# Kernel optimization log

Hardware: AMD Instinct MI355X
Metric: run time of the kernel (lower is better)

The kernel has to match this reference:

```python
import jax, jax.numpy as jnp
import numpy as np

F = 128      # n_features
NRBF = 6     # radial basis size
NSH = 7      # spherical basis size (SbfLayer(N_shbf, N_shbf, c))
NBIL = 8     # bilinear dim
CUT = 5.0    # cutoff c
NA = 4096    # atoms
NE = 65536   # edges
NT = 262144  # triplets
NB = 64      # molecules in batch
NZ = 95      # atom types


def _swish(x):
    return x * jax.nn.sigmoid(x)


def setup_inputs():
    key = jax.random.key(0)
    ks = list(jax.random.split(key, 32))
    def nrm(k, shape, s):
        return jax.random.normal(k, shape, dtype=jnp.float32) * s
    inp = {}
    inp['Z'] = jax.random.randint(ks[0], (NA,), 0, NZ)
    inp['R'] = jax.random.normal(ks[1], (NA, 3), dtype=jnp.float32)
    inp['batch_seg'] = jnp.sort(jax.random.randint(ks[2], (NA,), 0, NB))
    inp['idnb_i'] = jax.random.randint(ks[3], (NE,), 0, NA)
    inp['idnb_j'] = jax.random.randint(ks[4], (NE,), 0, NA)
    inp['id_expand_kj'] = jax.random.randint(ks[5], (NT,), 0, NE)
    inp['id_reduce_ji'] = jax.random.randint(ks[6], (NT,), 0, NE)
    inp['id3dnb_i'] = jax.random.randint(ks[7], (NT,), 0, NA)
    inp['id3dnb_j'] = jax.random.randint(ks[8], (NT,), 0, NA)
    inp['id3dnb_k'] = jax.random.randint(ks[9], (NT,), 0, NA)
    # learned parameters
    inp['emb'] = nrm(ks[10], (NZ, F), 0.1)
    inp['W_emb'] = nrm(ks[11], (2 * F + NRBF, F), 0.05)
    inp['b_emb'] = jnp.zeros((F,), jnp.float32)
    inp['out_Wrbf'] = nrm(ks[12], (8, NRBF, F), 0.05)
    inp['out_W1'] = nrm(ks[13], (8, F, F), 0.05)
    inp['out_b1'] = jnp.zeros((8, F), jnp.float32)
    inp['out_W2'] = nrm(ks[14], (8, F, 1), 0.05)
    inp['int_Wrbf'] = nrm(ks[15], (7, NRBF, F), 0.05)
    inp['int_Wsbf'] = nrm(ks[16], (7, NSH * NSH, NBIL), 0.05)
    inp['int_Wkj'] = nrm(ks[17], (7, F, F), 0.05)
    inp['int_bkj'] = jnp.zeros((7, F), jnp.float32)
    inp['int_Wji'] = nrm(ks[18], (7, F, F), 0.05)
    inp['int_bji'] = jnp.zeros((7, F), jnp.float32)
    inp['int_Wbil'] = nrm(ks[19], (7, F, NBIL, F), 0.02)
    inp['int_Wfin'] = nrm(ks[20], (7, F, F), 0.05)
    inp['int_bfin'] = jnp.zeros((7, F), jnp.float32)
    return inp


def _forward(Z, R, batch_seg, idnb_i, idnb_j, id_expand_kj, id_reduce_ji,
             id3dnb_i, id3dnb_j, id3dnb_k,
             emb, W_emb, b_emb,
             out_Wrbf, out_W1, out_b1, out_W2,
             int_Wrbf, int_Wsbf, int_Wkj, int_bkj, int_Wji, int_bji,
             int_Wbil, int_Wfin, int_bfin):
    n_atoms = Z.shape[0]
    n_edges = idnb_i.shape[0]
    # interatomic distances Dij [E]
    diff = R[idnb_i] - R[idnb_j]
    Dij = jnp.sqrt(jax.nn.relu(jnp.sum(diff * diff, -1)))
    dsafe = jnp.maximum(Dij, 1e-6)
    # radial Bessel basis [E, NRBF]
    n = jnp.arange(1, NRBF + 1, dtype=R.dtype)
    rbf = jnp.sqrt(2.0 / CUT) * jnp.sin(n * jnp.pi * dsafe[:, None] / CUT) / dsafe[:, None]
    # triplet angles via cross/atan2 [T]
    R1 = R[id3dnb_j] - R[id3dnb_i]
    R2 = R[id3dnb_k] - R[id3dnb_i]
    x = jnp.sum(R1 * R2, -1)
    y = jnp.linalg.norm(jnp.cross(R1, R2), axis=-1)
    ang = jnp.arctan2(y, x)
    # spherical basis: radial(d_kj) x angular(cos(l*theta)) -> [T, NSH*NSH]
    d_kj = jnp.maximum(Dij[id_expand_kj], 1e-6)
    nr = jnp.arange(1, NSH + 1, dtype=R.dtype)
    radial = jnp.sin(nr * jnp.pi * d_kj[:, None] / CUT) / d_kj[:, None]       # [T, NSH]
    ls = jnp.arange(NSH, dtype=R.dtype)
    angular = jnp.cos(ls[None, :] * ang[:, None])                              # [T, NSH]
    sbf = (angular[:, :, None] * radial[:, None, :]).reshape(ang.shape[0], NSH * NSH)
    # embedding: edge messages m [E, F]
    h = emb[Z]
    m = _swish(jnp.concatenate([h[idnb_i], h[idnb_j], rbf], -1) @ W_emb + b_emb)

    def out_layer(m, k):
        t = m * (rbf @ out_Wrbf[k])                                            # [E, F]
        ta = jax.ops.segment_sum(t, idnb_i, num_segments=n_atoms)             # [A, F]
        ta = _swish(ta @ out_W1[k] + out_b1[k])
        return ta @ out_W2[k]                                                  # [A, 1]

    P = out_layer(m, 0)
    for i in range(7):
        x_ji = _swish(m @ int_Wji[i] + int_bji[i])
        x_kj = _swish(m @ int_Wkj[i] + int_bkj[i]) * (rbf @ int_Wrbf[i])       # [E, F]
        x_kj = x_kj[id_expand_kj]                                              # [T, F]
        sb = sbf @ int_Wsbf[i]                                                 # [T, NBIL]
        x_kj = jnp.einsum('wl,wj,jli->wi', sb, x_kj, int_Wbil[i])             # [T, F]
        x_kj = jax.ops.segment_sum(x_kj, id_reduce_ji, num_segments=n_edges)  # [E, F]
        m = m + _swish((x_ji + x_kj) @ int_Wfin[i] + int_bfin[i])
        P = P + out_layer(m, i + 1)
    return jax.ops.segment_sum(P, batch_seg, num_segments=NB)                 # [NB, 1]


def reference(Z, R, batch_seg, idnb_i, idnb_j, id_expand_kj, id_reduce_ji,
              id3dnb_i, id3dnb_j, id3dnb_k,
              emb, W_emb, b_emb,
              out_Wrbf, out_W1, out_b1, out_W2,
              int_Wrbf, int_Wsbf, int_Wkj, int_bkj, int_Wji, int_bji,
              int_Wbil, int_Wfin, int_bfin):
    return _forward(Z, R, batch_seg, idnb_i, idnb_j, id_expand_kj, id_reduce_ji,
                    id3dnb_i, id3dnb_j, id3dnb_k,
                    emb, W_emb, b_emb,
                    out_Wrbf, out_W1, out_b1, out_W2,
                    int_Wrbf, int_Wsbf, int_Wkj, int_bkj, int_Wji, int_bji,
                    int_Wbil, int_Wfin, int_bfin)
```

## Files before the change

### kernel.cpp

```cpp
#include <hip/hip_runtime.h>

typedef __attribute__((ext_vector_type(8))) short shortx8;
typedef __attribute__((ext_vector_type(4))) float floatx4;

constexpr int NAc = 4096;
constexpr int NEc = 65536;
constexpr int NTc = 262144;
constexpr float PI_F = 3.14159265358979323846f;
constexpr float SQ25 = 0.63245553203367587f;

__device__ __forceinline__ float bf2f(unsigned short h){ return __uint_as_float(((unsigned)h)<<16); }
__device__ __forceinline__ unsigned short f2bf(float f){
  unsigned u = __float_as_uint(f);
  u += 0x7fffu + ((u>>16)&1u);
  return (unsigned short)(u>>16);
}
__device__ __forceinline__ float swishf(float x){ return x/(1.f+__expf(-x)); }

__device__ __forceinline__ floatx4 mfma16x16x32bf(shortx8 a, shortx8 b, floatx4 c){
  floatx4 d;
  asm("v_mfma_f32_16x16x32_bf16 %0, %1, %2, %3" : "=v"(d) : "v"(a), "v"(b), "v"(c));
  return d;
}

__global__ __launch_bounds__(256)
void egeom_k(const float* __restrict__ R, const int* __restrict__ ei,
             const int* __restrict__ ej, float* __restrict__ Dij, float* __restrict__ rbf){
  int e = blockIdx.x*256 + threadIdx.x;
  int i = ei[e], j = ej[e];
  float dx = R[i*3+0]-R[j*3+0];
  float dy = R[i*3+1]-R[j*3+1];
  float dz = R[i*3+2]-R[j*3+2];
  float d2 = dx*dx+dy*dy+dz*dz;
  float D = sqrtf(fmaxf(d2, 0.f));
  Dij[e] = D;
  float d = fmaxf(D, 1e-6f);
  float s = PI_F*d*0.2f;
  float sn, cs; sincosf(s, &sn, &cs);
  float invd = SQ25/d;
  float sprev = 0.f, scur = sn;
  #pragma unroll
  for (int q=0;q<6;q++){
    rbf[e*6+q] = scur*invd;
    float nx = 2.f*cs*scur - sprev; sprev = scur; scur = nx;
  }
}

__global__ __launch_bounds__(256)
void tgeom_k(const float* __restrict__ R, const int* __restrict__ t3i,
             const int* __restrict__ t3j, const int* __restrict__ t3k,
             const int* __restrict__ texp, const float* __restrict__ Dij,
             float* __restrict__ angrad){
  int w = blockIdx.x*256 + threadIdx.x;
  int ia = t3i[w], ja = t3j[w], ka = t3k[w];
  float xi = R[ia*3+0], yi = R[ia*3+1], zi = R[ia*3+2];
  float r1x = R[ja*3+0]-xi, r1y = R[ja*3+1]-yi, r1z = R[ja*3+2]-zi;
  float r2x = R[ka*3+0]-xi, r2y = R[ka*3+1]-yi, r2z = R[ka*3+2]-zi;
  float dt = r1x*r2x + r1y*r2y + r1z*r2z;
  float cx = r1y*r2z - r1z*r2y;
  float cy = r1z*r2x - r1x*r2z;
  float cz = r1x*r2y - r1y*r2x;
  float yv = sqrtf(cx*cx + cy*cy + cz*cz);
  float h = sqrtf(dt*dt + yv*yv);
  float c1 = (h > 0.f) ? dt/h : 1.f;
  angrad[0*NTc + w] = 1.f;
  angrad[1*NTc + w] = c1;
  float cprev = 1.f, ccur = c1;
  #pragma unroll
  for (int l=2;l<7;l++){
    float nx = 2.f*c1*ccur - cprev; cprev = ccur; ccur = nx;
    angrad[l*NTc + w] = nx;
  }
  float d = fmaxf(Dij[texp[w]], 1e-6f);
  float s = PI_F*d*0.2f;
  float sn, cs; sincosf(s, &sn, &cs);
  float invd = 1.f/d;
  float sprev = 0.f, scur = sn;
  #pragma unroll
  for (int q=0;q<7;q++){
    angrad[(7+q)*NTc + w] = scur*invd;
    float nx = 2.f*cs*scur - sprev; sprev = scur; scur = nx;
  }
}

__global__ __launch_bounds__(256)
void prep_transpose(const float* __restrict__ Wemb, const float* __restrict__ Wji,
                    const float* __restrict__ Wkj, const float* __restrict__ Wfin,
                    unsigned short* __restrict__ dW12, unsigned short* __restrict__ dWji,
                    unsigned short* __restrict__ dWkj, unsigned short* __restrict__ dWfin){
  int y = blockIdx.y;
  int x = blockIdx.x*256 + threadIdx.x;
  if (y == 0){
    if (x < 32768){
      int n = x >> 8, k = x & 255;
      dW12[x] = f2bf(Wemb[k*128 + n]);
    }
  } else {
    if (x < 16384){
      int n = x >> 7, k = x & 127;
      const float* s; unsigned short* d;
      if (y <= 7)      { s = Wji  + (y-1)*16384;  d = dWji  + (y-1)*16384; }
      else if (y <= 14){ s = Wkj  + (y-8)*16384;  d = dWkj  + (y-8)*16384; }
      else             { s = Wfin + (y-15)*16384; d = dWfin + (y-15)*16384; }
      d[x] = f2bf(s[k*128 + n]);
    }
  }
}

__global__ __launch_bounds__(256)
void prep_wbil(const float* __restrict__ Wbil, unsigned short* __restrict__ dst){
  int x = blockIdx.x*256 + threadIdx.x;
  if (x < 7*131072){
    int i = x >> 17; int rem = x & 131071;
    int o = rem >> 10; int lj = rem & 1023;
    int l = lj >> 7; int j = lj & 127;
    dst[x] = f2bf(Wbil[(size_t)i*131072 + (size_t)(j*8+l)*128 + o]);
  }
}

__global__ __launch_bounds__(256)
void prep_emb(const float* __restrict__ emb, unsigned short* __restrict__ d){
  int x = blockIdx.x*256 + threadIdx.x;
  if (x < 95*128) d[x] = f2bf(emb[x]);
}

__global__ __launch_bounds__(256)
void hist_k(const int* __restrict__ ids, int n, int* __restrict__ hist){
  int stride = gridDim.x*blockDim.x;
  for (int x = blockIdx.x*blockDim.x + threadIdx.x; x < n; x += stride)
    atomicAdd(&hist[ids[x]], 1);
}

__global__ __launch_bounds__(1024)
void scan_k(const int* __restrict__ hist, int* __restrict__ offs, int nbins){
  __shared__ int part[1024];
  int tid = threadIdx.x;
  int per = nbins >> 10;
  int base = tid*per;
  int s = 0;
  for (int q=0;q<per;q++) s += hist[base+q];
  part[tid] = s;
  __syncthreads();
  for (int d=1; d<1024; d<<=1){
    int v = (tid>=d) ? part[tid-d] : 0;
    __syncthreads();
    part[tid] += v;
    __syncthreads();
  }
  int run = (tid>0) ? part[tid-1] : 0;
  for (int q=0;q<per;q++){ offs[base+q] = run; run += hist[base+q]; }
  if (tid==1023) offs[nbins] = part[1023];
}

__global__ __launch_bounds__(256)
void scatter_k(const int* __restrict__ ids, int n, const int* __restrict__ offs,
               int* __restrict__ cursor, int* __restrict__ perm){
  int stride = gridDim.x*blockDim.x;
  for (int x = blockIdx.x*blockDim.x + threadIdx.x; x < n; x += stride){
    int b = ids[x];
    int pos = offs[b] + atomicAdd(&cursor[b], 1);
    perm[pos] = x;
  }
}

__global__ __launch_bounds__(256)
void sb_k(const float* __restrict__ angrad, const float* __restrict__ Wsbf,
          float* __restrict__ sb){
  __shared__ float Ws[392];
  for (int x = threadIdx.x; x < 392; x += 256) Ws[x] = Wsbf[x];
  __syncthreads();
  int w = blockIdx.x*256 + threadIdx.x;
  float ca[7], rd[7];
  #pragma unroll
  for (int q=0;q<7;q++){ ca[q] = angrad[q*NTc + w]; rd[q] = angrad[(7+q)*NTc + w]; }
  float o[8] = {0,0,0,0,0,0,0,0};
  #pragma unroll
  for (int a=0;a<7;a++){
    #pragma unroll
    for (int r=0;r<7;r++){
      float pr = ca[a]*rd[r];
      const float* wp = &Ws[(a*7+r)*8];
      #pragma unroll
      for (int l=0;l<8;l++) o[l] += pr*wp[l];
    }
  }
  #pragma unroll
  for (int l=0;l<8;l++) sb[(size_t)w*8 + l] = o[l];
}

__global__ __launch_bounds__(256)
void gbuild_k(int c0, const int* __restrict__ tperm, const int* __restrict__ toffs,
              const int* __restrict__ texp, const float* __restrict__ sb,
              const unsigned short* __restrict__ xkj, unsigned short* __restrict__ G){
  int lane = threadIdx.x & 63;
  int wv = threadIdx.x >> 6;
  int r = c0 + blockIdx.x*4 + wv;
  float acc[8][2] = {};
  int s = toffs[r], e_ = toffs[r+1];
  for (int t = s; t < e_; t++){
    int wt = tperm[t];
    int e = texp[wt];
    unsigned xv = *(const unsigned*)&xkj[(size_t)e*128 + lane*2];
    float x0 = bf2f((unsigned short)(xv & 0xffffu));
    float x1 = bf2f((unsigned short)(xv >> 16));
    const float* sp = sb + (size_t)wt*8;
    #pragma unroll
    for (int l=0;l<8;l++){ float sl = sp[l]; acc[l][0] += sl*x0; acc[l][1] += sl*x1; }
  }
  size_t gb = (size_t)(r - c0)*1024 + lane*2;
  #pragma unroll
  for (int l=0;l<8;l++){
    unsigned pv = (unsigned)f2bf(acc[l][0]) | ((unsigned)f2bf(acc[l][1]) << 16);
    *(unsigned*)&G[gb + l*128] = pv;
  }
}

template<int MODE, int EPI>
__global__ __launch_bounds__(256)
void gemm_k(const unsigned short* __restrict__ A, const unsigned short* __restrict__ Bt,
            int K, int rowoff, int arow0,
            const int* __restrict__ gi, const int* __restrict__ gj, const int* __restrict__ Zr,
            const float* __restrict__ rbfp, const float* __restrict__ W6,
            const float* __restrict__ bias, const float* minp,
            const unsigned short* __restrict__ xjip,
            float* outF, unsigned short* outB){
  __shared__ __align__(16) unsigned short As[128*72];
  __shared__ __align__(16) unsigned short Bs[128*72];
  const int tid = threadIdx.x;
  const int lane = tid & 63;
  const int wid = tid >> 6;
  const int wr = wid >> 1, wc = wid & 1;
  const int rowbase = rowoff + blockIdx.x*128;
  floatx4 acc[4][4];
  #pragma unroll
  for (int i=0;i<4;i++)
    #pragma unroll
    for (int j=0;j<4;j++) acc[i][j] = (floatx4){0.f,0.f,0.f,0.f};

  for (int k0 = 0; k0 < K; k0 += 64){
    shortx8 ra[4], rb[4];
    #pragma unroll
    for (int q=0;q<4;q++){
      int c = q*256 + tid;
      int row = c >> 3;
      int ko = (c & 7) << 3;
      const unsigned short* asrc;
      if (MODE == 0){
        asrc = A + (size_t)(rowbase - arow0 + row)*K + k0 + ko;
      } else {
        int grow = rowbase + row;
        int kg = k0 + ko;
        int atom = (kg < 128) ? gi[grow] : gj[grow];
        asrc = A + (size_t)Zr[atom]*128 + (kg & 127);
      }
      ra[q] = *(const shortx8*)asrc;
      rb[q] = *(const shortx8*)(Bt + (size_t)row*K + k0 + ko);
    }
    __syncthreads();
    #pragma unroll
    for (int q=0;q<4;q++){
      int c = q*256 + tid;
      int row = c >> 3;
      int ko = (c & 7) << 3;
      *(shortx8*)&As[row*72 + ko] = ra[q];
      *(shortx8*)&Bs[row*72 + ko] = rb[q];
    }
    __syncthreads();
    #pragma unroll
    for (int kk=0; kk<2; kk++){
      shortx8 af[4], bfr[4];
      #pragma unroll
      for (int mi=0;mi<4;mi++)
        af[mi] = *(const shortx8*)&As[(wr*64 + mi*16 + (lane&15))*72 + kk*32 + ((lane>>4)<<3)];
      #pragma unroll
      for (int ni=0;ni<4;ni++)
        bfr[ni] = *(const shortx8*)&Bs[(wc*64 + ni*16 + (lane&15))*72 + kk*32 + ((lane>>4)<<3)];
      #pragma unroll
      for (int mi=0;mi<4;mi++)
        #pragma unroll
        for (int ni=0;ni<4;ni++)
          acc[mi][ni] = mfma16x16x32bf(af[mi], bfr[ni], acc[mi][ni]);
    }
  }
  asm volatile("s_nop 7\ns_nop 7\ns_nop 7");

  #pragma unroll
  for (int mi=0;mi<4;mi++){
    #pragma unroll
    for (int j=0;j<4;j++){
      int row = wr*64 + mi*16 + ((lane>>4)<<2) + j;
      int grow = rowbase + row;
      float rb6[6];
      if (EPI==0 || EPI==2){
        #pragma unroll
        for (int q=0;q<6;q++) rb6[q] = rbfp[grow*6+q];
      }
      #pragma unroll
      for (int ni=0;ni<4;ni++){
        int col = wc*64 + ni*16 + (lane&15);
        float v = acc[mi][ni][j];
        size_t oidx = (size_t)grow*128 + col;
        if (EPI==0){
          float e = bias[col];
          #pragma unroll
          for (int q=0;q<6;q++) e += rb6[q]*W6[q*128+col];
          v = swishf(v + e);
          outF[oidx] = v;
          outB[oidx] = f2bf(v);
        } else if (EPI==1){
          v = swishf(v + bias[col]);
          outB[oidx] = f2bf(v);
        } else if (EPI==2){
          float rp = 0.f;
          #pragma unroll
          for (int q=0;q<6;q++) rp += rb6[q]*W6[q*128+col];
          v = swishf(v + bias[col]) * rp;
          outB[oidx] = f2bf(v);
        } else if (EPI==3){
          v += bf2f(xjip[oidx]);
          outB[oidx] = f2bf(v);
        } else {
          float nm = minp[oidx] + swishf(v + bias[col]);
          outF[oidx] = nm;
          outB[oidx] = f2bf(nm);
        }
      }
    }
  }
}

__global__ __launch_bounds__(256)
void out_layer_k(const int* __restrict__ eperm, const int* __restrict__ eoffs,
                 const unsigned short* __restrict__ mbf, const float* __restrict__ rbf,
                 const float* __restrict__ Wrbf, const float* __restrict__ W1,
                 const float* __restrict__ b1, const float* __restrict__ W2,
                 const int* __restrict__ bseg, float* __restrict__ out){
  __shared__ float ta_lds[4][128];
  int lane = threadIdx.x & 63;
  int wv = threadIdx.x >> 6;
  int a = blockIdx.x*4 + wv;
  int f0 = lane*2;
  float wr0[6], wr1[6];
  #pragma unroll
  for (int q=0;q<6;q++){ wr0[q] = Wrbf[q*128+f0]; wr1[q] = Wrbf[q*128+f0+1]; }
  float ta0 = 0.f, ta1 = 0.f;
  int s = eoffs[a], e_ = eoffs[a+1];
  for (int t = s; t < e_; t++){
    int e = eperm[t];
    unsigned mv = *(const unsigned*)&mbf[(size_t)e*128 + f0];
    float r0 = rbf[e*6+0], r1 = rbf[e*6+1], r2 = rbf[e*6+2];
    float r3 = rbf[e*6+3], r4 = rbf[e*6+4], r5 = rbf[e*6+5];
    float rp0 = r0*wr0[0]+r1*wr0[1]+r2*wr0[2]+r3*wr0[3]+r4*wr0[4]+r5*wr0[5];
    float rp1 = r0*wr1[0]+r1*wr1[1]+r2*wr1[2]+r3*wr1[3]+r4*wr1[4]+r5*wr1[5];
    ta0 += bf2f((unsigned short)(mv & 0xffffu))*rp0;
    ta1 += bf2f((unsigned short)(mv >> 16))*rp1;
  }
  ta_lds[wv][f0]   = ta0;
  ta_lds[wv][f0+1] = ta1;
  float p = 0.f;
  #pragma unroll
  for (int h=0; h<2; h++){
    int n = lane + h*64;
    float o = b1[n];
    for (int f=0; f<128; f++) o += ta_lds[wv][f]*W1[f*128+n];
    p += swishf(o)*W2[n];
  }
  #pragma unroll
  for (int off=32; off; off>>=1) p += __shfl_down(p, off);
  if (lane == 0) atomicAdd(&out[bseg[a]], p);
}

extern "C" void kernel_launch(void* const* d_in, const int* in_sizes, int n_in,
                              void* d_out, int out_size, void* d_ws, size_t ws_size,
                              hipStream_t stream){
  const int*   Z    = (const int*)d_in[0];
  const float* R    = (const float*)d_in[1];
  const int*   bseg = (const int*)d_in[2];
  const int*   ei   = (const int*)d_in[3];
  const int*   ej   = (const int*)d_in[4];
  const int*   texp = (const int*)d_in[5];
  const int*   tred = (const int*)d_in[6];
  const int*   t3i  = (const int*)d_in[7];
  const int*   t3j  = (const int*)d_in[8];
  const int*   t3k  = (const int*)d_in[9];
  const float* emb  = (const float*)d_in[10];
  const float* Wemb = (const float*)d_in[11];
  const float* bemb = (const float*)d_in[12];
  const float* oWr  = (const float*)d_in[13];
  const float* oW1  = (const float*)d_in[14];
  const float* ob1  = (const float*)d_in[15];
  const float* oW2  = (const float*)d_in[16];
  const float* iWr  = (const float*)d_in[17];
  const float* iWs  = (const float*)d_in[18];
  const float* iWkj = (const float*)d_in[19];
  const float* ibkj = (const float*)d_in[20];
  const float* iWji = (const float*)d_in[21];
  const float* ibji = (const float*)d_in[22];
  const float* iWb  = (const float*)d_in[23];
  const float* iWf  = (const float*)d_in[24];
  const float* ibf  = (const float*)d_in[25];
  float* out = (float*)d_out;

  char* p = (char*)d_ws;
  auto alloc = [&](size_t bytes)->char*{ char* r = p; p += (bytes + 255) & ~(size_t)255; return r; };
  float* Dij    = (float*)alloc((size_t)NEc*4);
  float* rbf    = (float*)alloc((size_t)NEc*6*4);
  float* angrad = (float*)alloc((size_t)14*NTc*4);
  float* sball  = (float*)alloc((size_t)NTc*8*4);
  float* m      = (float*)alloc((size_t)NEc*128*4);
  unsigned short* mbf  = (unsigned short*)alloc((size_t)NEc*128*2);
  unsigned short* xji  = (unsigned short*)alloc((size_t)NEc*128*2);
  unsigned short* xkj  = (unsigned short*)alloc((size_t)NEc*128*2);
  unsigned short* afin = (unsigned short*)alloc((size_t)NEc*128*2);
  int* thist = (int*)alloc((size_t)NEc*4);
  int* toffs = (int*)alloc((size_t)(NEc+1)*4);
  int* tperm = (int*)alloc((size_t)NTc*4);
  int* ehist = (int*)alloc((size_t)NAc*4);
  int* eoffs = (int*)alloc((size_t)(NAc+1)*4);
  int* eperm = (int*)alloc((size_t)NEc*4);
  unsigned short* embbf = (unsigned short*)alloc((size_t)95*128*2);
  unsigned short* W12et = (unsigned short*)alloc((size_t)128*256*2);
  unsigned short* Wjit  = (unsigned short*)alloc((size_t)7*16384*2);
  unsigned short* Wkjt  = (unsigned short*)alloc((size_t)7*16384*2);
  unsigned short* Wfint = (unsigned short*)alloc((size_t)7*16384*2);
  unsigned short* Wbilt = (unsigned short*)alloc((size_t)7*131072*2);
  size_t fixed = (size_t)(p - (char*)d_ws);

  int nch = 1;
  while (nch < 8 && fixed + ((size_t)NEc/nch)*1024*2 > ws_size) nch <<= 1;
  int ECH = NEc / nch;
  unsigned short* Gbuf = (unsigned short*)alloc((size_t)ECH*1024*2);

  hipMemsetAsync(d_out, 0, 64*sizeof(float), stream);
  hipMemsetAsync(thist, 0, (size_t)NEc*4, stream);
  hipMemsetAsync(ehist, 0, (size_t)NAc*4, stream);

  prep_transpose<<<dim3(128,22),256,0,stream>>>(Wemb, iWji, iWkj, iWf, W12et, Wjit, Wkjt, Wfint);
  prep_wbil<<<3584,256,0,stream>>>(iWb, Wbilt);
  prep_emb<<<48,256,0,stream>>>(emb, embbf);
  egeom_k<<<NEc/256,256,0,stream>>>(R, ei, ej, Dij, rbf);
  tgeom_k<<<NTc/256,256,0,stream>>>(R, t3i, t3j, t3k, texp, Dij, angrad);

  hist_k<<<512,256,0,stream>>>(tred, NTc, thist);
  scan_k<<<1,1024,0,stream>>>(thist, toffs, NEc);
  hipMemsetAsync(thist, 0, (size_t)NEc*4, stream);
  scatter_k<<<512,256,0,stream>>>(tred, NTc, toffs, thist, tperm);
  hist_k<<<256,256,0,stream>>>(ei, NEc, ehist);
  scan_k<<<1,1024,0,stream>>>(ehist, eoffs, NAc);
  hipMemsetAsync(ehist, 0, (size_t)NAc*4, stream);
  scatter_k<<<256,256,0,stream>>>(ei, NEc, eoffs, ehist, eperm);

  gemm_k<1,0><<<NEc/128,256,0,stream>>>(embbf, W12et, 256, 0, 0, ei, ej, Z,
                                        rbf, Wemb + 256*128, bemb, nullptr, nullptr, m, mbf);
  out_layer_k<<<NAc/4,256,0,stream>>>(eperm, eoffs, mbf, rbf,
                                      oWr, oW1, ob1, oW2, bseg, out);

  for (int i=0;i<7;i++){
    sb_k<<<NTc/256,256,0,stream>>>(angrad, iWs + i*392, sball);
    gemm_k<0,1><<<NEc/128,256,0,stream>>>(mbf, Wjit + i*16384, 128, 0, 0,
        nullptr, nullptr, nullptr, nullptr, nullptr, ibji + i*128, nullptr, nullptr, nullptr, xji);
    gemm_k<0,2><<<NEc/128,256,0,stream>>>(mbf, Wkjt + i*16384, 128, 0, 0,
        nullptr, nullptr, nullptr, rbf, iWr + i*768, ibkj + i*128, nullptr, nullptr, nullptr, xkj);
    for (int c=0;c<nch;c++){
      int c0 = c*ECH;
      gbuild_k<<<ECH/4,256,0,stream>>>(c0, tperm, toffs, texp, sball, xkj, Gbuf);
      gemm_k<0,3><<<ECH/128,256,0,stream>>>(Gbuf, Wbilt + i*131072, 1024, c0, c0,
          nullptr, nullptr, nullptr, nullptr, nullptr, nullptr, nullptr, xji, nullptr, afin);
    }
    gemm_k<0,4><<<NEc/128,256,0,stream>>>(afin, Wfint + i*16384, 128, 0, 0,
        nullptr, nullptr, nullptr, nullptr, nullptr, ibf + i*128, m, nullptr, m, mbf);
    out_layer_k<<<NAc/4,256,0,stream>>>(eperm, eoffs, mbf, rbf,
        oWr + (i+1)*768, oW1 + (i+1)*16384, ob1 + (i+1)*128, oW2 + (i+1)*128, bseg, out);
  }
  (void)in_sizes; (void)n_in; (void)out_size;
}
```

Measured before the change: 1.789 ms.

## Pre-permute triplet data, merge ji/kj GEMMs, parallelize scan, vectorize gbuild stores

Triplet angular features and expand indices are gathered once into reduce-sorted order, so sb_k and gbuild_k read contiguously instead of through tperm indirection. The ji and kj projection GEMMs are merged into one launch with a 2D grid over a concatenated weight. The single-block scan is replaced by a three-kernel multi-block scan. The G layout changes to lane-contiguous 16-element vectors with matching Wbil reordering so stores are 128-bit. These target indirect gathers, launch count and serial scan cost, at the price of extra buffers and a one-time permutation pass.

Result: slower. 1.871 ms (+4.6%).

```diff
diff --git a/kernel.cpp b/kernel.cpp
--- a/kernel.cpp
+++ b/kernel.cpp
@@ -2,6 +2,7 @@
 
 typedef __attribute__((ext_vector_type(8))) short shortx8;
 typedef __attribute__((ext_vector_type(4))) float floatx4;
+typedef __attribute__((ext_vector_type(4))) unsigned uintx4;
 
 constexpr int NAc = 4096;
 constexpr int NEc = 65536;
@@ -86,8 +87,8 @@
 __global__ __launch_bounds__(256)
 void prep_transpose(const float* __restrict__ Wemb, const float* __restrict__ Wji,
                     const float* __restrict__ Wkj, const float* __restrict__ Wfin,
-                    unsigned short* __restrict__ dW12, unsigned short* __restrict__ dWji,
-                    unsigned short* __restrict__ dWkj, unsigned short* __restrict__ dWfin){
+                    unsigned short* __restrict__ dW12, unsigned short* __restrict__ dWjk,
+                    unsigned short* __restrict__ dWfin){
   int y = blockIdx.y;
   int x = blockIdx.x*256 + threadIdx.x;
   if (y == 0){
@@ -99,8 +100,8 @@
     if (x < 16384){
       int n = x >> 7, k = x & 127;
       const float* s; unsigned short* d;
-      if (y <= 7)      { s = Wji  + (y-1)*16384;  d = dWji  + (y-1)*16384; }
-      else if (y <= 14){ s = Wkj  + (y-8)*16384;  d = dWkj  + (y-8)*16384; }
+      if (y <= 7)      { s = Wji  + (y-1)*16384;  d = dWjk  + (y-1)*32768; }
+      else if (y <= 14){ s = Wkj  + (y-8)*16384;  d = dWjk  + (y-8)*32768 + 16384; }
       else             { s = Wfin + (y-15)*16384; d = dWfin + (y-15)*16384; }
       d[x] = f2bf(s[k*128 + n]);
     }
@@ -112,9 +113,8 @@
   int x = blockIdx.x*256 + threadIdx.x;
   if (x < 7*131072){
     int i = x >> 17; int rem = x & 131071;
-    int o = rem >> 10; int lj = rem & 1023;
-    int l = lj >> 7; int j = lj & 127;
-    dst[x] = f2bf(Wbil[(size_t)i*131072 + (size_t)(j*8+l)*128 + o]);
+    int o = rem >> 10; int k = rem & 1023;
+    dst[x] = f2bf(Wbil[(size_t)i*131072 + (size_t)k*128 + o]);
   }
 }
 
@@ -131,25 +131,43 @@
     atomicAdd(&hist[ids[x]], 1);
 }
 
-__global__ __launch_bounds__(1024)
-void scan_k(const int* __restrict__ hist, int* __restrict__ offs, int nbins){
-  __shared__ int part[1024];
-  int tid = threadIdx.x;
-  int per = nbins >> 10;
-  int base = tid*per;
-  int s = 0;
-  for (int q=0;q<per;q++) s += hist[base+q];
-  part[tid] = s;
-  __syncthreads();
-  for (int d=1; d<1024; d<<=1){
-    int v = (tid>=d) ? part[tid-d] : 0;
-    __syncthreads();
-    part[tid] += v;
-    __syncthreads();
-  }
-  int run = (tid>0) ? part[tid-1] : 0;
-  for (int q=0;q<per;q++){ offs[base+q] = run; run += hist[base+q]; }
-  if (tid==1023) offs[nbins] = part[1023];
+__global__ __launch_bounds__(256)
+void scan1_k(const int* __restrict__ hist, int* __restrict__ offs, int* __restrict__ bsum){
+  __shared__ int buf[256];
+  int t = threadIdx.x;
+  int x = blockIdx.x*256 + t;
+  int v = hist[x];
+  buf[t] = v; __syncthreads();
+  #pragma unroll
+  for (int d=1; d<256; d<<=1){
+    int u = (t>=d) ? buf[t-d] : 0;
+    __syncthreads(); buf[t] += u; __syncthreads();
+  }
+  offs[x] = buf[t] - v;
+  if (t == 255) bsum[blockIdx.x] = buf[255];
+}
+
+__global__ __launch_bounds__(256)
+void scan2_k(int* __restrict__ bsum, int nb){
+  __shared__ int buf[256];
+  int t = threadIdx.x;
+  int v = (t < nb) ? bsum[t] : 0;
+  buf[t] = v; __syncthreads();
+  #pragma unroll
+  for (int d=1; d<256; d<<=1){
+    int u = (t>=d) ? buf[t-d] : 0;
+    __syncthreads(); buf[t] += u; __syncthreads();
+  }
+  if (t < nb) bsum[t] = buf[t] - v;
+}
+
+__global__ __launch_bounds__(256)
+void scan3_k(const int* __restrict__ hist, int* __restrict__ offs,
+             const int* __restrict__ bsum, int nbins){
+  int x = blockIdx.x*256 + threadIdx.x;
+  int o = offs[x] + bsum[blockIdx.x];
+  offs[x] = o;
+  if (x == nbins-1) offs[nbins] = o + hist[x];
 }
 
 __global__ __launch_bounds__(256)
@@ -164,15 +182,27 @@
 }
 
 __global__ __launch_bounds__(256)
-void sb_k(const float* __restrict__ angrad, const float* __restrict__ Wsbf,
+void permt_k(const int* __restrict__ tperm, const int* __restrict__ texp,
+             const float* __restrict__ angrad, int* __restrict__ tmeta,
+             float* __restrict__ angp){
+  int p = blockIdx.x*256 + threadIdx.x;
+  int w = tperm[p];
+  tmeta[p] = texp[w];
+  #pragma unroll
+  for (int q=0;q<14;q++) angp[(size_t)p*16 + q] = angrad[q*NTc + w];
+}
+
+__global__ __launch_bounds__(256)
+void sb_k(const float* __restrict__ angp, const float* __restrict__ Wsbf,
           float* __restrict__ sb){
   __shared__ float Ws[392];
   for (int x = threadIdx.x; x < 392; x += 256) Ws[x] = Wsbf[x];
   __syncthreads();
-  int w = blockIdx.x*256 + threadIdx.x;
-  float ca[7], rd[7];
-  #pragma unroll
-  for (int q=0;q<7;q++){ ca[q] = angrad[q*NTc + w]; rd[q] = angrad[(7+q)*NTc + w]; }
+  int p = blockIdx.x*256 + threadIdx.x;
+  const float4* ap = (const float4*)(angp + (size_t)p*16);
+  float4 a0 = ap[0], a1 = ap[1], a2 = ap[2], a3 = ap[3];
+  float ca[7] = {a0.x,a0.y,a0.z,a0.w,a1.x,a1.y,a1.z};
+  float rd[7] = {a1.w,a2.x,a2.y,a2.z,a2.w,a3.x,a3.y};
   float o[8] = {0,0,0,0,0,0,0,0};
   #pragma unroll
   for (int a=0;a<7;a++){
@@ -184,35 +214,45 @@
       for (int l=0;l<8;l++) o[l] += pr*wp[l];
     }
   }
-  #pragma unroll
-  for (int l=0;l<8;l++) sb[(size_t)w*8 + l] = o[l];
-}
-
-__global__ __launch_bounds__(256)
-void gbuild_k(int c0, const int* __restrict__ tperm, const int* __restrict__ toffs,
-              const int* __restrict__ texp, const float* __restrict__ sb,
-              const unsigned short* __restrict__ xkj, unsigned short* __restrict__ G){
+  float4* op = (float4*)(sb + (size_t)p*8);
+  op[0] = (float4){o[0],o[1],o[2],o[3]};
+  op[1] = (float4){o[4],o[5],o[6],o[7]};
+}
+
+__global__ __launch_bounds__(256)
+void gbuild_k(int c0, const int* __restrict__ toffs, const int* __restrict__ tmeta,
+              const float* __restrict__ sb, const unsigned short* __restrict__ xkj,
+              unsigned short* __restrict__ G){
   int lane = threadIdx.x & 63;
-  int wv = threadIdx.x >> 6;
+  int wv = __builtin_amdgcn_readfirstlane(threadIdx.x >> 6);
   int r = c0 + blockIdx.x*4 + wv;
-  float acc[8][2] = {};
+  float acc0[8] = {}, acc1[8] = {};
   int s = toffs[r], e_ = toffs[r+1];
   for (int t = s; t < e_; t++){
-    int wt = tperm[t];
-    int e = texp[wt];
+    int e = tmeta[t];
     unsigned xv = *(const unsigned*)&xkj[(size_t)e*128 + lane*2];
+    float4 s0 = *(const float4*)&sb[(size_t)t*8];
+    float4 s1 = *(const float4*)&sb[(size_t)t*8 + 4];
     float x0 = bf2f((unsigned short)(xv & 0xffffu));
     float x1 = bf2f((unsigned short)(xv >> 16));
-    const float* sp = sb + (size_t)wt*8;
-    #pragma unroll
-    for (int l=0;l<8;l++){ float sl = sp[l]; acc[l][0] += sl*x0; acc[l][1] += sl*x1; }
-  }
-  size_t gb = (size_t)(r - c0)*1024 + lane*2;
-  #pragma unroll
-  for (int l=0;l<8;l++){
-    unsigned pv = (unsigned)f2bf(acc[l][0]) | ((unsigned)f2bf(acc[l][1]) << 16);
-    *(unsigned*)&G[gb + l*128] = pv;
-  }
+    acc0[0] += s0.x*x0; acc1[0] += s0.x*x1;
+    acc0[1] += s0.y*x0; acc1[1] += s0.y*x1;
+    acc0[2] += s0.z*x0; acc1[2] += s0.z*x1;
+    acc0[3] += s0.w*x0; acc1[3] += s0.w*x1;
+    acc0[4] += s1.x*x0; acc1[4] += s1.x*x1;
+    acc0[5] += s1.y*x0; acc1[5] += s1.y*x1;
+    acc0[6] += s1.z*x0; acc1[6] += s1.z*x1;
+    acc0[7] += s1.w*x0; acc1[7] += s1.w*x1;
+  }
+  size_t base = (size_t)(r - c0)*1024 + (size_t)lane*16;
+  uintx4 v0, v1;
+  #pragma unroll
+  for (int d=0; d<4; d++){
+    v0[d] = (unsigned)f2bf(acc0[2*d]) | ((unsigned)f2bf(acc0[2*d+1]) << 16);
+    v1[d] = (unsigned)f2bf(acc1[2*d]) | ((unsigned)f2bf(acc1[2*d+1]) << 16);
+  }
+  *(uintx4*)&G[base]     = v0;
+  *(uintx4*)&G[base + 8] = v1;
 }
 
 template<int MODE, int EPI>
@@ -221,9 +261,9 @@
             int K, int rowoff, int arow0,
             const int* __restrict__ gi, const int* __restrict__ gj, const int* __restrict__ Zr,
             const float* __restrict__ rbfp, const float* __restrict__ W6,
-            const float* __restrict__ bias, const float* minp,
-            const unsigned short* __restrict__ xjip,
-            float* outF, unsigned short* outB){
+            const float* __restrict__ bias, const float* __restrict__ bias2,
+            const float* minp, const unsigned short* __restrict__ xjip,
+            float* outF, unsigned short* outB, unsigned short* outB2){
   __shared__ __align__(16) unsigned short As[128*72];
   __shared__ __align__(16) unsigned short Bs[128*72];
   const int tid = threadIdx.x;
@@ -231,6 +271,7 @@
   const int wid = tid >> 6;
   const int wr = wid >> 1, wc = wid & 1;
   const int rowbase = rowoff + blockIdx.x*128;
+  const int brow0 = (EPI==5) ? (int)blockIdx.y*128 : 0;
   floatx4 acc[4][4];
   #pragma unroll
   for (int i=0;i<4;i++)
@@ -254,7 +295,7 @@
         asrc = A + (size_t)Zr[atom]*128 + (kg & 127);
       }
       ra[q] = *(const shortx8*)asrc;
-      rb[q] = *(const shortx8*)(Bt + (size_t)row*K + k0 + ko);
+      rb[q] = *(const shortx8*)(Bt + (size_t)(brow0 + row)*K + k0 + ko);
     }
     __syncthreads();
     #pragma unroll
@@ -291,7 +332,8 @@
       int row = wr*64 + mi*16 + ((lane>>4)<<2) + j;
       int grow = rowbase + row;
       float rb6[6];
-      if (EPI==0 || EPI==2){
+      bool needr = (EPI==0) || ((EPI==5) && blockIdx.y==1);
+      if (needr){
         #pragma unroll
         for (int q=0;q<6;q++) rb6[q] = rbfp[grow*6+q];
       }
@@ -307,22 +349,24 @@
           v = swishf(v + e);
           outF[oidx] = v;
           outB[oidx] = f2bf(v);
-        } else if (EPI==1){
-          v = swishf(v + bias[col]);
-          outB[oidx] = f2bf(v);
-        } else if (EPI==2){
-          float rp = 0.f;
-          #pragma unroll
-          for (int q=0;q<6;q++) rp += rb6[q]*W6[q*128+col];
-          v = swishf(v + bias[col]) * rp;
-          outB[oidx] = f2bf(v);
         } else if (EPI==3){
           v += bf2f(xjip[oidx]);
           outB[oidx] = f2bf(v);
-        } else {
+        } else if (EPI==4){
           float nm = minp[oidx] + swishf(v + bias[col]);
           outF[oidx] = nm;
           outB[oidx] = f2bf(nm);
+        } else {
+          if (blockIdx.y == 0){
+            v = swishf(v + bias[col]);
+            outB[oidx] = f2bf(v);
+          } else {
+            float rp = 0.f;
+            #pragma unroll
+            for (int q=0;q<6;q++) rp += rb6[q]*W6[q*128+col];
+            v = swishf(v + bias2[col]) * rp;
+            outB2[oidx] = f2bf(v);
+          }
         }
       }
     }
@@ -337,7 +381,7 @@
                  const int* __restrict__ bseg, float* __restrict__ out){
   __shared__ float ta_lds[4][128];
   int lane = threadIdx.x & 63;
-  int wv = threadIdx.x >> 6;
+  int wv = __builtin_amdgcn_readfirstlane(threadIdx.x >> 6);
   int a = blockIdx.x*4 + wv;
   int f0 = lane*2;
   float wr0[6], wr1[6];
@@ -406,6 +450,7 @@
   float* Dij    = (float*)alloc((size_t)NEc*4);
   float* rbf    = (float*)alloc((size_t)NEc*6*4);
   float* angrad = (float*)alloc((size_t)14*NTc*4);
+  float* angp   = (float*)alloc((size_t)NTc*16*4);
   float* sball  = (float*)alloc((size_t)NTc*8*4);
   float* m      = (float*)alloc((size_t)NEc*128*4);
   unsigned short* mbf  = (unsigned short*)alloc((size_t)NEc*128*2);
@@ -415,13 +460,14 @@
   int* thist = (int*)alloc((size_t)NEc*4);
   int* toffs = (int*)alloc((size_t)(NEc+1)*4);
   int* tperm = (int*)alloc((size_t)NTc*4);
+  int* tmeta = (int*)alloc((size_t)NTc*4);
   int* ehist = (int*)alloc((size_t)NAc*4);
   int* eoffs = (int*)alloc((size_t)(NAc+1)*4);
   int* eperm = (int*)alloc((size_t)NEc*4);
+  int* bsum  = (int*)alloc((size_t)257*4);
   unsigned short* embbf = (unsigned short*)alloc((size_t)95*128*2);
   unsigned short* W12et = (unsigned short*)alloc((size_t)128*256*2);
-  unsigned short* Wjit  = (unsigned short*)alloc((size_t)7*16384*2);
-  unsigned short* Wkjt  = (unsigned short*)alloc((size_t)7*16384*2);
+  unsigned short* Wjkt  = (unsigned short*)alloc((size_t)7*32768*2);
   unsigned short* Wfint = (unsigned short*)alloc((size_t)7*16384*2);
   unsigned short* Wbilt = (unsigned short*)alloc((size_t)7*131072*2);
   size_t fixed = (size_t)(p - (char*)d_ws);
@@ -435,40 +481,46 @@
   hipMemsetAsync(thist, 0, (size_t)NEc*4, stream);
   hipMemsetAsync(ehist, 0, (size_t)NAc*4, stream);
 
-  prep_transpose<<<dim3(128,22),256,0,stream>>>(Wemb, iWji, iWkj, iWf, W12et, Wjit, Wkjt, Wfint);
+  prep_transpose<<<dim3(128,22),256,0,stream>>>(Wemb, iWji, iWkj, iWf, W12et, Wjkt, Wfint);
   prep_wbil<<<3584,256,0,stream>>>(iWb, Wbilt);
   prep_emb<<<48,256,0,stream>>>(emb, embbf);
   egeom_k<<<NEc/256,256,0,stream>>>(R, ei, ej, Dij, rbf);
   tgeom_k<<<NTc/256,256,0,stream>>>(R, t3i, t3j, t3k, texp, Dij, angrad);
 
   hist_k<<<512,256,0,stream>>>(tred, NTc, thist);
-  scan_k<<<1,1024,0,stream>>>(thist, toffs, NEc);
+  scan1_k<<<NEc/256,256,0,stream>>>(thist, toffs, bsum);
+  scan2_k<<<1,256,0,stream>>>(bsum, NEc/256);
+  scan3_k<<<NEc/256,256,0,stream>>>(thist, toffs, bsum, NEc);
   hipMemsetAsync(thist, 0, (size_t)NEc*4, stream);
   scatter_k<<<512,256,0,stream>>>(tred, NTc, toffs, thist, tperm);
   hist_k<<<256,256,0,stream>>>(ei, NEc, ehist);
-  scan_k<<<1,1024,0,stream>>>(ehist, eoffs, NAc);
+  scan1_k<<<NAc/256,256,0,stream>>>(ehist, eoffs, bsum);
+  scan2_k<<<1,256,0,stream>>>(bsum, NAc/256);
+  scan3_k<<<NAc/256,256,0,stream>>>(ehist, eoffs, bsum, NAc);
   hipMemsetAsync(ehist, 0, (size_t)NAc*4, stream);
   scatter_k<<<256,256,0,stream>>>(ei, NEc, eoffs, ehist, eperm);
+  permt_k<<<NTc/256,256,0,stream>>>(tperm, texp, angrad, tmeta, angp);
 
   gemm_k<1,0><<<NEc/128,256,0,stream>>>(embbf, W12et, 256, 0, 0, ei, ej, Z,
-                                        rbf, Wemb + 256*128, bemb, nullptr, nullptr, m, mbf);
+      rbf, Wemb + 256*128, bemb, nullptr, nullptr, nullptr, m, mbf, nullptr);
   out_layer_k<<<NAc/4,256,0,stream>>>(eperm, eoffs, mbf, rbf,
                                       oWr, oW1, ob1, oW2, bseg, out);
 
   for (int i=0;i<7;i++){
-    sb_k<<<NTc/256,256,0,stream>>>(angrad, iWs + i*392, sball);
-    gemm_k<0,1><<<NEc/128,256,0,stream>>>(mbf, Wjit + i*16384, 128, 0, 0,
-        nullptr, nullptr, nullptr, nullptr, nullptr, ibji + i*128, nullptr, nullptr, nullptr, xji);
-    gemm_k<0,2><<<NEc/128,256,0,stream>>>(mbf, Wkjt + i*16384, 128, 0, 0,
-        nullptr, nullptr, nullptr, rbf, iWr + i*768, ibkj + i*128, nullptr, nullptr, nullptr, xkj);
+    sb_k<<<NTc/256,256,0,stream>>>(angp, iWs + i*392, sball);
+    gemm_k<0,5><<<dim3(NEc/128,2),256,0,stream>>>(mbf, Wjkt + i*32768, 128, 0, 0,
+        nullptr, nullptr, nullptr, rbf, iWr + i*768, ibji + i*128, ibkj + i*128,
+        nullptr, nullptr, nullptr, xji, xkj);
     for (int c=0;c<nch;c++){
       int c0 = c*ECH;
-      gbuild_k<<<ECH/4,256,0,stream>>>(c0, tperm, toffs, texp, sball, xkj, Gbuf);
+      gbuild_k<<<ECH/4,256,0,stream>>>(c0, toffs, tmeta, sball, xkj, Gbuf);
       gemm_k<0,3><<<ECH/128,256,0,stream>>>(Gbuf, Wbilt + i*131072, 1024, c0, c0,
-          nullptr, nullptr, nullptr, nullptr, nullptr, nullptr, nullptr, xji, nullptr, afin);
+          nullptr, nullptr, nullptr, nullptr, nullptr, nullptr, nullptr, nullptr,
+          xji, nullptr, afin, nullptr);
     }
     gemm_k<0,4><<<NEc/128,256,0,stream>>>(afin, Wfint + i*16384, 128, 0, 0,
-        nullptr, nullptr, nullptr, nullptr, nullptr, ibf + i*128, m, nullptr, m, mbf);
+        nullptr, nullptr, nullptr, nullptr, nullptr, ibf + i*128, nullptr,
+        m, nullptr, m, mbf, nullptr);
     out_layer_k<<<NAc/4,256,0,stream>>>(eperm, eoffs, mbf, rbf,
         oWr + (i+1)*768, oW1 + (i+1)*16384, ob1 + (i+1)*128, oW2 + (i+1)*128, bseg, out);
   }
```
